# Optimization experiments

Hardware: AMD Instinct MI355X
Metric: run time of the kernel (lower is better)

Reference implementation:

```python
import jax, jax.numpy as jnp
import numpy as np

EPS = 1e-5

def setup_inputs() -> dict:
    key = jax.random.key(0)
    ks = jax.random.split(key, 9)
    B, C, H, W = 64, 256, 64, 64
    HID = 16
    def lin_init(k, fan_in, shape):
        bound = 1.0 / np.sqrt(fan_in)
        return jax.random.uniform(k, shape, jnp.float32, -bound, bound)
    return {
        "x": jax.random.normal(ks[0], (B, C, H, W), jnp.float32),
        # fc_mean: Linear(2,16) -> ReLU -> Linear(16,1) -> Sigmoid
        "wm1": lin_init(ks[1], 2, (HID, 2)),
        "bm1": lin_init(ks[2], 2, (HID,)),
        "wm2": lin_init(ks[3], HID, (1, HID)),
        "bm2": lin_init(ks[4], HID, (1,)),
        # fc_std: same architecture
        "ws1": lin_init(ks[5], 2, (HID, 2)),
        "bs1": lin_init(ks[6], 2, (HID,)),
        "ws2": lin_init(ks[7], HID, (1, HID)),
        "bs2": lin_init(ks[8], HID, (1,)),
    }

def _mlp(stats, w1, b1, w2, b2):
    # stats: [B, C, 2] -> [B, C] sigmoid gate
    h = jax.nn.relu(jnp.einsum("bci,hi->bch", stats, w1) + b1)
    return jax.nn.sigmoid(jnp.einsum("bch,oh->bco", h, w2) + b2)[..., 0]

def reference(x, wm1, bm1, wm2, bm2, ws1, bs1, ws2, bs2):
    # Eval-mode CNSN: CrossNorm is identity (not training); apply SelfNorm.
    mean = jnp.mean(x, axis=(2, 3))                       # [B, C]
    var = jnp.var(x, axis=(2, 3), ddof=1)                 # unbiased, as torch.var
    std = jnp.sqrt(var + EPS)                             # [B, C]
    stats = jnp.stack([mean, std], axis=-1)               # [B, C, 2]
    mean_w = _mlp(stats, wm1, bm1, wm2, bm2)              # [B, C]
    std_w = _mlp(stats, ws1, bs1, ws2, bs2)               # [B, C]
    m = mean[:, :, None, None]
    s = std[:, :, None, None]
    x_norm = (x - m) / s
    return x_norm * (s * std_w[:, :, None, None]) + m * mean_w[:, :, None, None]
```

## Files before the change

### kernel.cpp

```cpp
#include <hip/hip_runtime.h>
#include <math.h>

#define EPSV 1e-5f
#define HW   4096
#define NBC  16384

__global__ __launch_bounds__(256) void cnsn_fused(
    const float* __restrict__ x,
    const float* __restrict__ wm1, const float* __restrict__ bm1,
    const float* __restrict__ wm2, const float* __restrict__ bm2,
    const float* __restrict__ ws1, const float* __restrict__ bs1,
    const float* __restrict__ ws2, const float* __restrict__ bs2,
    float* __restrict__ out)
{
    const int bc = blockIdx.x;
    const size_t base = (size_t)bc * HW;
    const float4* __restrict__ xp4 = (const float4*)(x + base);
    float4*       __restrict__ op4 = (float4*)(out + base);
    const int tid = threadIdx.x;

    float4 v[4];
    float sum = 0.f, sumsq = 0.f;
    #pragma unroll
    for (int it = 0; it < 4; ++it) {
        v[it] = xp4[tid + it * 256];
        sum   += v[it].x + v[it].y + v[it].z + v[it].w;
        sumsq += v[it].x*v[it].x + v[it].y*v[it].y
               + v[it].z*v[it].z + v[it].w*v[it].w;
    }

    #pragma unroll
    for (int off = 32; off > 0; off >>= 1) {
        sum   += __shfl_down(sum,   off, 64);
        sumsq += __shfl_down(sumsq, off, 64);
    }
    __shared__ float s_sum[4], s_sq[4];
    __shared__ float s_ab[2];
    const int wave = tid >> 6;
    if ((tid & 63) == 0) { s_sum[wave] = sum; s_sq[wave] = sumsq; }
    __syncthreads();

    if (tid == 0) {
        const float S = s_sum[0] + s_sum[1] + s_sum[2] + s_sum[3];
        const float Q = s_sq[0]  + s_sq[1]  + s_sq[2]  + s_sq[3];
        const float N = (float)HW;
        const float mean = S / N;
        const float var  = (Q - S * mean) / (N - 1.0f);
        const float stdv = sqrtf(var + EPSV);

        float accm = bm2[0];
        #pragma unroll
        for (int h = 0; h < 16; ++h) {
            float hv = fmaf(wm1[h*2+0], mean, fmaf(wm1[h*2+1], stdv, bm1[h]));
            accm = fmaf(wm2[h], fmaxf(hv, 0.f), accm);
        }
        const float mw = 1.f / (1.f + expf(-accm));

        float accs = bs2[0];
        #pragma unroll
        for (int h = 0; h < 16; ++h) {
            float hv = fmaf(ws1[h*2+0], mean, fmaf(ws1[h*2+1], stdv, bs1[h]));
            accs = fmaf(ws2[h], fmaxf(hv, 0.f), accs);
        }
        const float sw = 1.f / (1.f + expf(-accs));

        s_ab[0] = sw;
        s_ab[1] = mean * (mw - sw);
    }
    __syncthreads();

    const float a = s_ab[0];
    const float b = s_ab[1];
    #pragma unroll
    for (int it = 0; it < 4; ++it) {
        float4 o;
        o.x = fmaf(v[it].x, a, b);
        o.y = fmaf(v[it].y, a, b);
        o.z = fmaf(v[it].z, a, b);
        o.w = fmaf(v[it].w, a, b);
        op4[tid + it * 256] = o;
    }
}

extern "C" void kernel_launch(void* const* d_in, const int* in_sizes, int n_in,
                              void* d_out, int out_size, void* d_ws, size_t ws_size,
                              hipStream_t stream) {
    const float* x   = (const float*)d_in[0];
    const float* wm1 = (const float*)d_in[1];
    const float* bm1 = (const float*)d_in[2];
    const float* wm2 = (const float*)d_in[3];
    const float* bm2 = (const float*)d_in[4];
    const float* ws1 = (const float*)d_in[5];
    const float* bs1 = (const float*)d_in[6];
    const float* ws2 = (const float*)d_in[7];
    const float* bs2 = (const float*)d_in[8];
    float* out = (float*)d_out;

    cnsn_fused<<<NBC, 256, 0, stream>>>(x, wm1, bm1, wm2, bm2,
                                        ws1, bs1, ws2, bs2, out);
}
```

Measured before the change: 100.3 us.

## Assign one wave per channel and use nontemporal loads and stores

Each 64-lane wave now handles a whole (b,c) plane, holding 16 float4 values per lane, so four channels are processed per block. The reduction becomes a butterfly shuffle within the wave, which removes the shared-memory stage, both block barriers and the serial tid==0 MLP step; every lane now evaluates the small MLP itself. Loads and stores use nontemporal hints to avoid polluting the cache on this streaming workload. The cost is higher register pressure (64 floats per lane) and fewer independent blocks.

```diff
diff --git a/kernel.cpp b/kernel.cpp
--- a/kernel.cpp
+++ b/kernel.cpp
@@ -4,8 +4,11 @@
 #define EPSV 1e-5f
 #define HW   4096
 #define NBC  16384
+#define WPB  4
 
-__global__ __launch_bounds__(256) void cnsn_fused(
+typedef float vf4 __attribute__((ext_vector_type(4)));
+
+__global__ __launch_bounds__(256) void cnsn_fused_wave(
     const float* __restrict__ x,
     const float* __restrict__ wm1, const float* __restrict__ bm1,
     const float* __restrict__ wm2, const float* __restrict__ bm2,
@@ -13,17 +16,18 @@
     const float* __restrict__ ws2, const float* __restrict__ bs2,
     float* __restrict__ out)
 {
-    const int bc = blockIdx.x;
+    const int wave = threadIdx.x >> 6;
+    const int lane = threadIdx.x & 63;
+    const int bc   = blockIdx.x * WPB + wave;
     const size_t base = (size_t)bc * HW;
-    const float4* __restrict__ xp4 = (const float4*)(x + base);
-    float4*       __restrict__ op4 = (float4*)(out + base);
-    const int tid = threadIdx.x;
+    const vf4* __restrict__ xp4 = (const vf4*)(x + base);
+    vf4*       __restrict__ op4 = (vf4*)(out + base);
 
-    float4 v[4];
+    vf4 v[16];
     float sum = 0.f, sumsq = 0.f;
     #pragma unroll
-    for (int it = 0; it < 4; ++it) {
-        v[it] = xp4[tid + it * 256];
+    for (int it = 0; it < 16; ++it) {
+        v[it] = __builtin_nontemporal_load(&xp4[lane + it * 64]);
         sum   += v[it].x + v[it].y + v[it].z + v[it].w;
         sumsq += v[it].x*v[it].x + v[it].y*v[it].y
                + v[it].z*v[it].z + v[it].w*v[it].w;
@@ -31,54 +35,42 @@
 
     #pragma unroll
     for (int off = 32; off > 0; off >>= 1) {
-        sum   += __shfl_down(sum,   off, 64);
-        sumsq += __shfl_down(sumsq, off, 64);
+        sum   += __shfl_xor(sum,   off, 64);
+        sumsq += __shfl_xor(sumsq, off, 64);
     }
-    __shared__ float s_sum[4], s_sq[4];
-    __shared__ float s_ab[2];
-    const int wave = tid >> 6;
-    if ((tid & 63) == 0) { s_sum[wave] = sum; s_sq[wave] = sumsq; }
-    __syncthreads();
 
-    if (tid == 0) {
-        const float S = s_sum[0] + s_sum[1] + s_sum[2] + s_sum[3];
-        const float Q = s_sq[0]  + s_sq[1]  + s_sq[2]  + s_sq[3];
-        const float N = (float)HW;
-        const float mean = S / N;
-        const float var  = (Q - S * mean) / (N - 1.0f);
-        const float stdv = sqrtf(var + EPSV);
+    const float N    = (float)HW;
+    const float mean = sum / N;
+    const float var  = (sumsq - sum * mean) / (N - 1.0f);
+    const float stdv = sqrtf(var + EPSV);
 
-        float accm = bm2[0];
-        #pragma unroll
-        for (int h = 0; h < 16; ++h) {
-            float hv = fmaf(wm1[h*2+0], mean, fmaf(wm1[h*2+1], stdv, bm1[h]));
-            accm = fmaf(wm2[h], fmaxf(hv, 0.f), accm);
-        }
-        const float mw = 1.f / (1.f + expf(-accm));
+    float accm = bm2[0];
+    #pragma unroll
+    for (int h = 0; h < 16; ++h) {
+        float hv = fmaf(wm1[h*2+0], mean, fmaf(wm1[h*2+1], stdv, bm1[h]));
+        accm = fmaf(wm2[h], fmaxf(hv, 0.f), accm);
+    }
+    const float mw = 1.f / (1.f + expf(-accm));
 
-        float accs = bs2[0];
-        #pragma unroll
-        for (int h = 0; h < 16; ++h) {
-            float hv = fmaf(ws1[h*2+0], mean, fmaf(ws1[h*2+1], stdv, bs1[h]));
-            accs = fmaf(ws2[h], fmaxf(hv, 0.f), accs);
-        }
-        const float sw = 1.f / (1.f + expf(-accs));
+    float accs = bs2[0];
+    #pragma unroll
+    for (int h = 0; h < 16; ++h) {
+        float hv = fmaf(ws1[h*2+0], mean, fmaf(ws1[h*2+1], stdv, bs1[h]));
+        accs = fmaf(ws2[h], fmaxf(hv, 0.f), accs);
+    }
+    const float sw = 1.f / (1.f + expf(-accs));
 
-        s_ab[0] = sw;
-        s_ab[1] = mean * (mw - sw);
-    }
-    __syncthreads();
+    const float a = sw;
+    const float b = mean * (mw - sw);
 
-    const float a = s_ab[0];
-    const float b = s_ab[1];
     #pragma unroll
-    for (int it = 0; it < 4; ++it) {
-        float4 o;
+    for (int it = 0; it < 16; ++it) {
+        vf4 o;
         o.x = fmaf(v[it].x, a, b);
         o.y = fmaf(v[it].y, a, b);
         o.z = fmaf(v[it].z, a, b);
         o.w = fmaf(v[it].w, a, b);
-        op4[tid + it * 256] = o;
+        __builtin_nontemporal_store(o, &op4[lane + it * 64]);
     }
 }
 
@@ -96,6 +88,6 @@
     const float* bs2 = (const float*)d_in[8];
     float* out = (float*)d_out;
 
-    cnsn_fused<<<NBC, 256, 0, stream>>>(x, wm1, bm1, wm2, bm2,
-                                        ws1, bs1, ws2, bs2, out);
+    cnsn_fused_wave<<<NBC / WPB, 256, 0, stream>>>(x, wm1, bm1, wm2, bm2,
+                                                   ws1, bs1, ws2, bs2, out);
 }
```

Result: faster. 96.41 us (-3.9%).
